# Kernel optimization log

Measured on AMD Instinct MI355X. Metric: run time of the kernel, lower is better.

## Reference

```python
import jax, jax.numpy as jnp
import numpy as np

D_MODEL = 1024
H = 16
D_K = D_MODEL // H
MAX_SEQ_LEN = 2048
B = 2
S = 2048


def setup_inputs() -> dict:
    key = jax.random.key(0)
    ks = jax.random.split(key, 8)
    scale = 1.0 / np.sqrt(D_MODEL)
    return {
        "q": jax.random.normal(ks[0], (B, S, D_MODEL), jnp.float32),
        "k": jax.random.normal(ks[1], (B, S, D_MODEL), jnp.float32),
        "v": jax.random.normal(ks[2], (B, S, D_MODEL), jnp.float32),
        "mask": jnp.ones((B, 1, S, S), dtype=bool),
        "w_q": jax.random.normal(ks[3], (D_MODEL, D_MODEL), jnp.float32) * scale,
        "w_k": jax.random.normal(ks[4], (D_MODEL, D_MODEL), jnp.float32) * scale,
        "w_v": jax.random.normal(ks[5], (D_MODEL, D_MODEL), jnp.float32) * scale,
        "w_o": jax.random.normal(ks[6], (D_MODEL, D_MODEL), jnp.float32) * scale,
        "rel_emb": jax.random.normal(ks[7], (2 * MAX_SEQ_LEN - 1, H), jnp.float32) * 0.02,
    }


def reference(q, k, v, mask, w_q, w_k, w_v, w_o, rel_emb):
    batch, seq_len, _ = q.shape
    # projections (nn.Linear without bias: x @ W.T)
    query = (q @ w_q.T).reshape(batch, seq_len, H, D_K).transpose(0, 2, 1, 3)
    key_ = (k @ w_k.T).reshape(batch, seq_len, H, D_K).transpose(0, 2, 1, 3)
    value = (v @ w_v.T).reshape(batch, seq_len, H, D_K).transpose(0, 2, 1, 3)
    # scores: [B, H, S, S]
    scores = jnp.einsum("bhqd,bhkd->bhqk", query, key_) / jnp.sqrt(jnp.float32(D_K))
    # relative position bias
    rng = jnp.arange(seq_len)
    rel_pos = rng[:, None] - rng[None, :] + (MAX_SEQ_LEN - 1)  # [S, S]
    rel_bias = rel_emb[rel_pos]                                # [S, S, H]
    scores = scores + rel_bias.transpose(2, 0, 1)[None]        # [1, H, S, S]
    scores = jnp.where(mask, scores, -1e9)
    attn = jax.nn.softmax(scores, axis=-1)  # dropout p=0 -> identity
    x = jnp.einsum("bhqk,bhkd->bhqd", attn, value)
    x = x.transpose(0, 2, 1, 3).reshape(batch, seq_len, H * D_K)
    return x @ w_o.T
```

## Files before the change

kernel.cpp:

```cpp
#include <hip/hip_runtime.h>
#include <hip/hip_bf16.h>
#include <stdint.h>

typedef __bf16 bf16_t;
typedef __bf16 bf16x8 __attribute__((ext_vector_type(8)));
typedef __bf16 bf16x4 __attribute__((ext_vector_type(4)));
typedef short  s16x4  __attribute__((ext_vector_type(4)));
typedef float  f32x4  __attribute__((ext_vector_type(4)));

#define D_MODEL 1024
#define NH 16
#define DK 64
#define SEQ 2048
#define BATCH 2
#define NKT (SEQ / 64)
#define LOG2E 1.44269504f

typedef const __attribute__((address_space(1))) void gas_void;
typedef __attribute__((address_space(3))) void las_void;
__device__ __forceinline__ void async16(const void* g, void* l) {
  __builtin_amdgcn_global_load_lds((gas_void*)g, (las_void*)l, 16, 0, 0);
}

__device__ __forceinline__ bf16x8 load8(const float* p) {
  float4 a = *(const float4*)p;
  float4 b = *(const float4*)(p + 4);
  bf16x8 r;
  r[0] = (bf16_t)a.x; r[1] = (bf16_t)a.y; r[2] = (bf16_t)a.z; r[3] = (bf16_t)a.w;
  r[4] = (bf16_t)b.x; r[5] = (bf16_t)b.y; r[6] = (bf16_t)b.z; r[7] = (bf16_t)b.w;
  return r;
}
__device__ __forceinline__ bf16x8 load8(const bf16_t* p) {
  return *(const bf16x8*)p;
}

__device__ __forceinline__ f32x4 mfma16x16x16_bf16(bf16x4 a, bf16x4 b, f32x4 c) {
#if __has_builtin(__builtin_amdgcn_mfma_f32_16x16x16_bf16)
  return __builtin_amdgcn_mfma_f32_16x16x16_bf16(a, b, c, 0, 0, 0);
#else
  union { bf16x4 h; s16x4 s; } ua, ub;
  ua.h = a; ub.h = b;
  return __builtin_amdgcn_mfma_f32_16x16x16bf16_1k(ua.s, ub.s, c, 0, 0, 0);
#endif
}

__global__ __launch_bounds__(256) void wcvt_kernel(
    const float* __restrict__ w0, const float* __restrict__ w1,
    const float* __restrict__ w2, const float* __restrict__ w3,
    bf16_t* __restrict__ o0, bf16_t* __restrict__ o1,
    bf16_t* __restrict__ o2, bf16_t* __restrict__ o3)
{
  const float* s; bf16_t* d;
  switch (blockIdx.y) {
    case 0:  s = w0; d = o0; break;
    case 1:  s = w1; d = o1; break;
    case 2:  s = w2; d = o2; break;
    default: s = w3; d = o3; break;
  }
  size_t i = (size_t)(blockIdx.x * 256 + threadIdx.x) * 8;
  *(bf16x8*)(d + i) = load8(s + i);
}

__global__ __launch_bounds__(256) void copy_kernel(
    const bf16_t* __restrict__ s, bf16_t* __restrict__ d)
{
  size_t i = (size_t)(blockIdx.x * 256 + threadIdx.x) * 8;
  *(bf16x8*)(d + i) = *(const bf16x8*)(s + i);
}

template <typename TA, typename TW>
__device__ __forceinline__ void gemm_mainloop_sync(const TA* __restrict__ A,
                                                   const TW* __restrict__ W,
                                                   int n0, int j0,
                                                   bf16_t* As, bf16_t* Ws,
                                                   f32x4 acc[4][4])
{
  const int tid  = threadIdx.x;
  const int wave = tid >> 6, lane = tid & 63;
  const int g = lane >> 4, rl = lane & 15;
  const int wm = (wave & 1) * 64, wn = (wave >> 1) * 64;

  for (int kt = 0; kt < D_MODEL / 64; ++kt) {
    __syncthreads();
#pragma unroll
    for (int i = 0; i < 4; ++i) {
      int c = tid + i * 256;
      int row = c >> 3, t = c & 7;
      *(bf16x8*)(As + row * 72 + t * 8) =
          load8(A + (size_t)(n0 + row) * D_MODEL + kt * 64 + t * 8);
      *(bf16x8*)(Ws + row * 72 + t * 8) =
          load8(W + (size_t)(j0 + row) * D_MODEL + kt * 64 + t * 8);
    }
    __syncthreads();
#pragma unroll
    for (int kc = 0; kc < 2; ++kc) {
      bf16x8 af[4], bfr[4];
#pragma unroll
      for (int mi = 0; mi < 4; ++mi)
        af[mi] = *(const bf16x8*)(As + (wm + mi * 16 + rl) * 72 + kc * 32 + g * 8);
#pragma unroll
      for (int ni = 0; ni < 4; ++ni)
        bfr[ni] = *(const bf16x8*)(Ws + (wn + ni * 16 + rl) * 72 + kc * 32 + g * 8);
#pragma unroll
      for (int mi = 0; mi < 4; ++mi)
#pragma unroll
        for (int ni = 0; ni < 4; ++ni)
          acc[mi][ni] = __builtin_amdgcn_mfma_f32_16x16x32_bf16(
              af[mi], bfr[ni], acc[mi][ni], 0, 0, 0);
    }
  }
}

__device__ __forceinline__ void qkv_epilogue(int which, int n0, int j0,
                                             f32x4 acc[4][4],
                                             bf16_t* qh, bf16_t* kh, bf16_t* vt)
{
  const int tid  = threadIdx.x;
  const int wave = tid >> 6, lane = tid & 63;
  const int g = lane >> 4, rl = lane & 15;
  const int wm = (wave & 1) * 64, wn = (wave >> 1) * 64;

  if (which == 2) {
    const int b = n0 >> 11;
#pragma unroll
    for (int mi = 0; mi < 4; ++mi)
#pragma unroll
      for (int ni = 0; ni < 4; ++ni) {
        bf16x4 pk;
#pragma unroll
        for (int r = 0; r < 4; ++r) pk[r] = (bf16_t)acc[mi][ni][r];
        int s = (n0 & (SEQ - 1)) + wm + mi * 16 + g * 4;
        int j = j0 + wn + ni * 16 + rl;
        int h = j >> 6, d = j & (DK - 1);
        int kl = s & 63;
        int n = ((kl >> 2) & 3) * 16 + ((kl >> 4) << 2);
        *(bf16x4*)(vt + ((((size_t)(b * NH + h) * NKT + (s >> 6)) * DK + d) << 6)
                   + n) = pk;
      }
  } else {
    bf16_t* O = (which == 0) ? qh : kh;
#pragma unroll
    for (int mi = 0; mi < 4; ++mi)
#pragma unroll
      for (int ni = 0; ni < 4; ++ni)
#pragma unroll
        for (int r = 0; r < 4; ++r) {
          int n = n0 + wm + mi * 16 + g * 4 + r;
          int j = j0 + wn + ni * 16 + rl;
          int b = n >> 11, s = n & (SEQ - 1);
          int h = j >> 6,  d = j & (DK - 1);
          O[((size_t)(b * NH + h) * SEQ + s) * DK + d] = (bf16_t)acc[mi][ni][r];
        }
  }
}

__global__ __launch_bounds__(256) void qkv_gemm_db2(
    const float* __restrict__ q, const float* __restrict__ k,
    const float* __restrict__ v,
    const bf16_t* __restrict__ wq, const bf16_t* __restrict__ wk,
    const bf16_t* __restrict__ wv,
    bf16_t* __restrict__ qh, bf16_t* __restrict__ kh, bf16_t* __restrict__ vt)
{
  __shared__ __align__(16) bf16_t smem[32768];

  const int bid   = blockIdx.x;
  const int lane8 = bid / 96;
  const int grp   = bid % 96;
  const int which = grp >> 5;
  const int nt    = grp & 31;
  const int j0 = lane8 * 128, n0 = nt * 128;

  const float*  A = (which == 0) ? q : (which == 1) ? k : v;
  const bf16_t* W = (which == 0) ? wq : (which == 1) ? wk : wv;

  const int tid  = threadIdx.x;
  const int wave = tid >> 6, lane = tid & 63;
  const int g = lane >> 4, rl = lane & 15;
  const int wm = (wave & 1) * 64, wn = (wave >> 1) * 64;
  const int row_ = tid >> 3, t_ = tid & 7;
  const int src_ = (t_ ^ (row_ & 7)) << 3;

  f32x4 pa[4], pb[4];
  f32x4 acc[4][4] = {};

  auto LOADA = [&](int kt) {
#pragma unroll
    for (int i = 0; i < 4; ++i) {
      const float* p = A + (size_t)(n0 + row_ + 32 * i) * D_MODEL + kt * 64 + t_ * 8;
      pa[i] = *(const f32x4*)p;
      pb[i] = *(const f32x4*)(p + 4);
    }
  };
  auto DMAW = [&](int kt, bf16_t* Wsb) {
#pragma unroll
    for (int i = 0; i < 4; ++i) {
      async16(W + (size_t)(j0 + row_ + 32 * i) * D_MODEL + kt * 64 + src_,
              Wsb + (tid + i * 256) * 8);
    }
  };
  auto WRITEA = [&](bf16_t* Asb) {
#pragma unroll
    for (int i = 0; i < 4; ++i) {
      bf16x8 h8;
#pragma unroll
      for (int r = 0; r < 4; ++r) {
        h8[r]     = (bf16_t)pa[i][r];
        h8[4 + r] = (bf16_t)pb[i][r];
      }
      *(bf16x8*)(Asb + (row_ + 32 * i) * 64 + src_) = h8;
    }
  };

  LOADA(0);
  DMAW(0, smem + 16384);
  WRITEA(smem);

  for (int kt = 0; kt < D_MODEL / 64; ++kt) {
    const int cur = kt & 1;
    if (kt + 1 < D_MODEL / 64) {
      LOADA(kt + 1);
      DMAW(kt + 1, smem + 16384 + (cur ^ 1) * 8192);
      asm volatile("s_waitcnt vmcnt(12) lgkmcnt(0)" ::: "memory");
    } else {
      asm volatile("s_waitcnt vmcnt(0) lgkmcnt(0)" ::: "memory");
    }
    __builtin_amdgcn_s_barrier();
    asm volatile("" ::: "memory");

    const bf16_t* Ab = smem + cur * 8192;
    const bf16_t* Wb = smem + 16384 + cur * 8192;
#pragma unroll
    for (int kc = 0; kc < 2; ++kc) {
      bf16x8 af[4], bfr[4];
      const int j8 = ((kc * 4 + g) ^ (rl & 7)) << 3;
#pragma unroll
      for (int mi = 0; mi < 4; ++mi)
        af[mi] = *(const bf16x8*)(Ab + (wm + mi * 16 + rl) * 64 + j8);
#pragma unroll
      for (int ni = 0; ni < 4; ++ni)
        bfr[ni] = *(const bf16x8*)(Wb + (wn + ni * 16 + rl) * 64 + j8);
      __builtin_amdgcn_s_setprio(1);
#pragma unroll
      for (int mi = 0; mi < 4; ++mi)
#pragma unroll
        for (int ni = 0; ni < 4; ++ni)
          acc[mi][ni] = __builtin_amdgcn_mfma_f32_16x16x32_bf16(
              af[mi], bfr[ni], acc[mi][ni], 0, 0, 0);
      __builtin_amdgcn_s_setprio(0);
    }

    if (kt + 1 < D_MODEL / 64) WRITEA(smem + (cur ^ 1) * 8192);
    asm volatile("s_waitcnt lgkmcnt(0)" ::: "memory");
    __builtin_amdgcn_s_barrier();
    asm volatile("" ::: "memory");
  }

  if (which == 2) {
    qkv_epilogue(2, n0, j0, acc, qh, kh, vt);
  } else {
    const int b = n0 >> 11, s0 = n0 & (SEQ - 1);
    bf16_t* O = (which == 0) ? qh : kh;
    __syncthreads();
    bf16_t* T = smem;
#pragma unroll
    for (int mi = 0; mi < 4; ++mi)
#pragma unroll
      for (int ni = 0; ni < 4; ++ni)
#pragma unroll
        for (int r = 0; r < 4; ++r)
          T[(wm + mi * 16 + g * 4 + r) * 136 + wn + ni * 16 + rl] =
              (bf16_t)acc[mi][ni][r];
    __syncthreads();
#pragma unroll
    for (int i = 0; i < 8; ++i) {
      int cc = tid + i * 256;
      int row = cc >> 4, t = cc & 15;
      int j = j0 + t * 8;
      int h = j >> 6, d = j & (DK - 1);
      *(bf16x8*)(O + ((size_t)(b * NH + h) * SEQ + s0 + row) * DK + d) =
          *(const bf16x8*)(T + row * 136 + t * 8);
    }
  }
}

__global__ __launch_bounds__(256) void qkv_gemm_sync(
    const float* __restrict__ q, const float* __restrict__ k,
    const float* __restrict__ v,
    const float* __restrict__ wq, const float* __restrict__ wk,
    const float* __restrict__ wv,
    bf16_t* __restrict__ qh, bf16_t* __restrict__ kh, bf16_t* __restrict__ vt)
{
  __shared__ __align__(16) bf16_t As[128 * 72];
  __shared__ __align__(16) bf16_t Ws[128 * 72];
  const int jt = blockIdx.x, nt = blockIdx.y;
  const int which = jt >> 3;
  const int j0 = (jt & 7) * 128, n0 = nt * 128;
  const float* A = (which == 0) ? q : (which == 1) ? k : v;
  const float* W = (which == 0) ? wq : (which == 1) ? wk : wv;
  f32x4 acc[4][4] = {};
  gemm_mainloop_sync(A, W, n0, j0, As, Ws, acc);
  qkv_epilogue(which, n0, j0, acc, qh, kh, vt);
}

__global__ __launch_bounds__(256) void attn_kernel(
    const bf16_t* __restrict__ qh, const bf16_t* __restrict__ kh,
    const bf16_t* __restrict__ vt, const float* __restrict__ rel,
    bf16_t* __restrict__ xa)
{
  __shared__ __align__(16) bf16_t Ks[2][4096];
  __shared__ __align__(16) bf16_t Vs[2][4096];
  __shared__ float relw[2176];

  const int bx = blockIdx.x;
  const int hb = bx & 31;
  const int qt = bx >> 5;
  const int h  = hb & (NH - 1);
  const int b  = hb >> 4;
  const int q0 = qt * 128;

  const size_t headoff = (size_t)(b * NH + h) * SEQ * DK;
  const bf16_t* Q  = qh + headoff;
  const bf16_t* K  = kh + headoff;
  const bf16_t* Vg = vt + headoff;

  const int tid  = threadIdx.x;
  const int wave = tid >> 6, lane = tid & 63;
  const int g = lane >> 4, rl = lane & 15;

  for (int t = tid; t < 2175; t += 256)
    relw[t] = rel[(size_t)(q0 + t) * NH + h] * LOG2E;

  bf16x8 aq[2][2];
#pragma unroll
  for (int mb = 0; mb < 2; ++mb) {
    const int qrow = q0 + wave * 32 + mb * 16 + rl;
    aq[mb][0] = *(const bf16x8*)(Q + (size_t)qrow * DK + g * 8);
    aq[mb][1] = *(const bf16x8*)(Q + (size_t)qrow * DK + 32 + g * 8);
  }

  bf16x4 ones4;
#pragma unroll
  for (int r = 0; r < 4; ++r) ones4[r] = (bf16_t)1.0f;

  f32x4 ls[2];
  ls[0] = (f32x4){0.f, 0.f, 0.f, 0.f};
  ls[1] = (f32x4){0.f, 0.f, 0.f, 0.f};
  f32x4 o[2][4];
#pragma unroll
  for (int mb = 0; mb < 2; ++mb)
#pragma unroll
    for (int nb = 0; nb < 4; ++nb) o[mb][nb] = (f32x4){0.f, 0.f, 0.f, 0.f};

  auto STAGE = [&](const bf16_t* Kt, const bf16_t* Vt, bf16_t* Kd, bf16_t* Vd) {
#pragma unroll
    for (int i = 0; i < 2; ++i) {
      int c = tid + i * 256;
      int pr  = c >> 7;
      int ph  = (c >> 6) & 1;
      int pg  = (c >> 4) & 3;
      int prl = c & 15;
      async16(Kt + (pr * 16 + prl) * 64 + ph * 32 + pg * 8, Kd + c * 8);
      async16(Vt + (pr * 16 + prl) * 64 + pg * 16 + ph * 8, Vd + c * 8);
    }
  };

  __syncthreads();

  STAGE(K, Vg, &Ks[0][0], &Vs[0][0]);

  for (int kt = 0; kt < NKT; ++kt) {
    const int cur = kt & 1;
    if (kt + 1 < NKT) {
      STAGE(K + (size_t)(kt + 1) * 4096, Vg + (size_t)(kt + 1) * 4096,
            &Ks[cur ^ 1][0], &Vs[cur ^ 1][0]);
      asm volatile("s_waitcnt vmcnt(4)" ::: "memory");
    } else {
      asm volatile("s_waitcnt vmcnt(0)" ::: "memory");
    }
    __builtin_amdgcn_s_barrier();
    asm volatile("" ::: "memory");

    const bf16_t* Kb = &Ks[cur][0];
    const bf16_t* Vb = &Vs[cur][0];

    bf16x8 kb0[4], kb1[4];
#pragma unroll
    for (int cb = 0; cb < 4; ++cb) {
      kb0[cb] = *(const bf16x8*)(Kb + (cb * 2 + 0) * 512 + lane * 8);
      kb1[cb] = *(const bf16x8*)(Kb + (cb * 2 + 1) * 512 + lane * 8);
    }
    bf16x8 vvf[4][2];
#pragma unroll
    for (int nb = 0; nb < 4; ++nb)
#pragma unroll
      for (int hf = 0; hf < 2; ++hf)
        vvf[nb][hf] = *(const bf16x8*)(Vb + (nb * 2 + hf) * 512 + lane * 8);

    const int base0 = wave * 32 + rl - g * 4 - kt * 64 + 2047;
    float rvw[5][4];
#pragma unroll
    for (int t5 = 0; t5 < 5; ++t5)
#pragma unroll
      for (int r = 0; r < 4; ++r)
        rvw[t5][r] = relw[base0 + (t5 - 3) * 16 - r];

    bf16x4 pf[2][4];
#pragma unroll
    for (int mb = 0; mb < 2; ++mb)
#pragma unroll
      for (int cb = 0; cb < 4; ++cb) {
        f32x4 a = (f32x4){0.f, 0.f, 0.f, 0.f};
        a = __builtin_amdgcn_mfma_f32_16x16x32_bf16(kb0[cb], aq[mb][0], a, 0, 0, 0);
        a = __builtin_amdgcn_mfma_f32_16x16x32_bf16(kb1[cb], aq[mb][1], a, 0, 0, 0);
        bf16x4 pk;
#pragma unroll
        for (int r = 0; r < 4; ++r)
          pk[r] = (bf16_t)__builtin_amdgcn_exp2f(
              fmaf(a[r], 0.125f * LOG2E, rvw[mb - cb + 3][r]));
        pf[mb][cb] = pk;
        ls[mb] = mfma16x16x16_bf16(pk, ones4, ls[mb]);
      }

    __builtin_amdgcn_s_setprio(1);
#pragma unroll
    for (int mb = 0; mb < 2; ++mb)
#pragma unroll
      for (int nb = 0; nb < 4; ++nb)
#pragma unroll
        for (int cb = 0; cb < 4; ++cb) {
          bf16x8 vv = vvf[nb][cb >> 1];
          bf16x4 v4;
#pragma unroll
          for (int r = 0; r < 4; ++r) v4[r] = vv[(cb & 1) * 4 + r];
          o[mb][nb] = mfma16x16x16_bf16(pf[mb][cb], v4, o[mb][nb]);
        }
    __builtin_amdgcn_s_setprio(0);

    __builtin_amdgcn_s_barrier();
  }

  float w2[2][4];
#pragma unroll
  for (int mb = 0; mb < 2; ++mb)
#pragma unroll
    for (int r = 0; r < 4; ++r) w2[mb][r] = 1.f / ls[mb][r];

#pragma unroll
  for (int mb = 0; mb < 2; ++mb)
#pragma unroll
    for (int nb = 0; nb < 4; ++nb)
#pragma unroll
      for (int r = 0; r < 4; ++r) {
        const int srow = q0 + wave * 32 + mb * 16 + g * 4 + r;
        const int d = nb * 16 + rl;
        xa[(size_t)(b * SEQ + srow) * D_MODEL + h * DK + d] =
            (bf16_t)(o[mb][nb][r] * w2[mb][r]);
      }
}

__device__ __forceinline__ void stage_out(
    const bf16_t* __restrict__ xa, const bf16_t* __restrict__ wo,
    int n0, int j0, int kt, bf16_t* Asb, bf16_t* Wsb, int tid)
{
#pragma unroll
  for (int i = 0; i < 2; ++i) {
    int c = tid + i * 256;
    int row = c >> 3, t = c & 7;
    int src = (t ^ (row & 7)) << 3;
    async16(xa + (size_t)(n0 + row) * D_MODEL + kt * 64 + src, Asb + c * 8);
  }
#pragma unroll
  for (int i = 0; i < 4; ++i) {
    int c = tid + i * 256;
    int row = c >> 3, t = c & 7;
    int src = (t ^ (row & 7)) << 3;
    async16(wo + (size_t)(j0 + row) * D_MODEL + kt * 64 + src, Wsb + c * 8);
  }
}

__global__ __launch_bounds__(256) void out_gemm_db(
    const bf16_t* __restrict__ xa, const bf16_t* __restrict__ wo,
    float* __restrict__ out)
{
  __shared__ __align__(16) bf16_t smem[24576];
  bf16_t* As = smem;
  bf16_t* Ws = smem + 8192;
  const int j0 = blockIdx.x * 128, n0 = blockIdx.y * 64;

  const int tid  = threadIdx.x;
  const int wave = tid >> 6, lane = tid & 63;
  const int g = lane >> 4, rl = lane & 15;
  const int wm = (wave & 1) * 32, wn = (wave >> 1) * 64;

  f32x4 acc[2][4] = {};
  stage_out(xa, wo, n0, j0, 0, As, Ws, tid);

  for (int kt = 0; kt < D_MODEL / 64; ++kt) {
    const int cur = kt & 1;
    if (kt + 1 < D_MODEL / 64) {
      stage_out(xa, wo, n0, j0, kt + 1, As + (cur ^ 1) * 4096,
                Ws + (cur ^ 1) * 8192, tid);
      asm volatile("s_waitcnt vmcnt(6)" ::: "memory");
    } else {
      asm volatile("s_waitcnt vmcnt(0)" ::: "memory");
    }
    __builtin_amdgcn_s_barrier();
    asm volatile("" ::: "memory");

    const bf16_t* Ab = As + cur * 4096;
    const bf16_t* Wb = Ws + cur * 8192;
#pragma unroll
    for (int kc = 0; kc < 2; ++kc) {
      bf16x8 af[2], bfr[4];
      const int j8 = ((kc * 4 + g) ^ (rl & 7)) << 3;
#pragma unroll
      for (int mi = 0; mi < 2; ++mi)
        af[mi] = *(const bf16x8*)(Ab + (wm + mi * 16 + rl) * 64 + j8);
#pragma unroll
      for (int ni = 0; ni < 4; ++ni)
        bfr[ni] = *(const bf16x8*)(Wb + (wn + ni * 16 + rl) * 64 + j8);
      __builtin_amdgcn_s_setprio(1);
#pragma unroll
      for (int mi = 0; mi < 2; ++mi)
#pragma unroll
        for (int ni = 0; ni < 4; ++ni)
          acc[mi][ni] = __builtin_amdgcn_mfma_f32_16x16x32_bf16(
              af[mi], bfr[ni], acc[mi][ni], 0, 0, 0);
      __builtin_amdgcn_s_setprio(0);
    }
    __builtin_amdgcn_s_barrier();
  }

#pragma unroll
  for (int mi = 0; mi < 2; ++mi)
#pragma unroll
    for (int ni = 0; ni < 4; ++ni)
#pragma unroll
      for (int r = 0; r < 4; ++r) {
        int n = n0 + wm + mi * 16 + g * 4 + r;
        int j = j0 + wn + ni * 16 + rl;
        out[(size_t)n * D_MODEL + j] = acc[mi][ni][r];
      }
}

__global__ __launch_bounds__(256) void out_gemm_sync(
    const bf16_t* __restrict__ xa, const float* __restrict__ wo,
    float* __restrict__ out)
{
  __shared__ __align__(16) bf16_t As[128 * 72];
  __shared__ __align__(16) bf16_t Ws[128 * 72];
  const int j0 = blockIdx.x * 128, n0 = blockIdx.y * 128;
  f32x4 acc[4][4] = {};
  gemm_mainloop_sync(xa, wo, n0, j0, As, Ws, acc);

  const int tid  = threadIdx.x;
  const int wave = tid >> 6, lane = tid & 63;
  const int g = lane >> 4, rl = lane & 15;
  const int wm = (wave & 1) * 64, wn = (wave >> 1) * 64;
#pragma unroll
  for (int mi = 0; mi < 4; ++mi)
#pragma unroll
    for (int ni = 0; ni < 4; ++ni)
#pragma unroll
      for (int r = 0; r < 4; ++r) {
        int n = n0 + wm + mi * 16 + g * 4 + r;
        int j = j0 + wn + ni * 16 + rl;
        out[(size_t)n * D_MODEL + j] = acc[mi][ni][r];
      }
}

extern "C" void kernel_launch(void* const* d_in, const int* in_sizes, int n_in,
                              void* d_out, int out_size, void* d_ws, size_t ws_size,
                              hipStream_t stream)
{
  const float* q   = (const float*)d_in[0];
  const float* k   = (const float*)d_in[1];
  const float* v   = (const float*)d_in[2];
  const float* wq  = (const float*)d_in[4];
  const float* wk  = (const float*)d_in[5];
  const float* wv  = (const float*)d_in[6];
  const float* wo  = (const float*)d_in[7];
  const float* rel = (const float*)d_in[8];
  float* out = (float*)d_out;

  char* ws = (char*)d_ws;
  const size_t seg  = (size_t)BATCH * SEQ * D_MODEL * sizeof(bf16_t);
  const size_t wseg = (size_t)D_MODEL * D_MODEL * sizeof(bf16_t);
  const size_t need = 4 * seg;

  if (ws_size >= need) {
    bf16_t* qh  = (bf16_t*)(ws);
    bf16_t* kh  = (bf16_t*)(ws + seg);
    bf16_t* vt  = (bf16_t*)(ws + 2 * seg);
    bf16_t* xa  = (bf16_t*)(ws + 3 * seg);
    bf16_t* wqb = (bf16_t*)d_out;
    bf16_t* wkb = (bf16_t*)((char*)d_out + wseg);
    bf16_t* wvb = (bf16_t*)((char*)d_out + 2 * wseg);
    bf16_t* wob = (bf16_t*)((char*)d_out + 3 * wseg);
    bf16_t* wos = qh;

    wcvt_kernel<<<dim3(512, 4), 256, 0, stream>>>(wq, wk, wv, wo,
                                                  wqb, wkb, wvb, wob);
    qkv_gemm_db2<<<dim3(768), 256, 0, stream>>>(q, k, v, wqb, wkb, wvb,
                                                qh, kh, vt);
    attn_kernel<<<dim3(512), 256, 0, stream>>>(qh, kh, vt, rel, xa);
    copy_kernel<<<dim3(512), 256, 0, stream>>>(wob, wos);
    out_gemm_db<<<dim3(8, 64), 256, 0, stream>>>(xa, wos, out);
  } else {
    bf16_t* qh = (bf16_t*)(ws);
    bf16_t* kh = (bf16_t*)(ws + seg);
    bf16_t* vt = (bf16_t*)(ws + 2 * seg);
    bf16_t* xa = (bf16_t*)(ws + 3 * seg);
    qkv_gemm_sync<<<dim3(24, 32), 256, 0, stream>>>(q, k, v, wq, wk, wv,
                                                    qh, kh, vt);
    attn_kernel<<<dim3(512), 256, 0, stream>>>(qh, kh, vt, rel, xa);
    out_gemm_sync<<<dim3(8, 32), 256, 0, stream>>>(xa, wo, out);
  }
}
```

Before: 247.6 us.

## Split attention key tiles across two waves per query group with LDS reduction

The attention kernel now runs 512 threads per block: each pair of waves shares a 32-row query group, and each wave in the pair handles half of every 64-key tile (intra-tile split-K). The partial output accumulators and row sums from the second wave go through shared memory (aliased onto the K/V buffers) and are added by the first wave before normalisation and store. This doubles the waves available for latency hiding and halves per-wave register use and MFMA work per tile. In exchange it adds two block-wide syncs and an LDS reduction at the end, and only half of the waves write output.

```diff
diff --git a/kernel.cpp b/kernel.cpp
--- a/kernel.cpp
+++ b/kernel.cpp
@@ -302,14 +302,16 @@
   qkv_epilogue(which, n0, j0, acc, qh, kh, vt);
 }
 
-__global__ __launch_bounds__(256) void attn_kernel(
+__global__ __launch_bounds__(512, 4) void attn_kernel(
     const bf16_t* __restrict__ qh, const bf16_t* __restrict__ kh,
     const bf16_t* __restrict__ vt, const float* __restrict__ rel,
     bf16_t* __restrict__ xa)
 {
-  __shared__ __align__(16) bf16_t Ks[2][4096];
-  __shared__ __align__(16) bf16_t Vs[2][4096];
-  __shared__ float relw[2176];
+  __shared__ __align__(16) char smem[41472];
+  bf16_t* Ks   = (bf16_t*)smem;
+  bf16_t* Vs   = (bf16_t*)(smem + 16384);
+  float*  relw = (float*)(smem + 32768);
+  float*  comb = (float*)smem;
 
   const int bx = blockIdx.x;
   const int hb = bx & 31;
@@ -324,16 +326,17 @@
   const bf16_t* Vg = vt + headoff;
 
   const int tid  = threadIdx.x;
-  const int wave = tid >> 6, lane = tid & 63;
+  const int w    = tid >> 6, lane = tid & 63;
+  const int qw   = w >> 1, kw = w & 1;
   const int g = lane >> 4, rl = lane & 15;
 
-  for (int t = tid; t < 2175; t += 256)
+  for (int t = tid; t < 2175; t += 512)
     relw[t] = rel[(size_t)(q0 + t) * NH + h] * LOG2E;
 
   bf16x8 aq[2][2];
 #pragma unroll
   for (int mb = 0; mb < 2; ++mb) {
-    const int qrow = q0 + wave * 32 + mb * 16 + rl;
+    const int qrow = q0 + qw * 32 + mb * 16 + rl;
     aq[mb][0] = *(const bf16x8*)(Q + (size_t)qrow * DK + g * 8);
     aq[mb][1] = *(const bf16x8*)(Q + (size_t)qrow * DK + 32 + g * 8);
   }
@@ -352,72 +355,68 @@
     for (int nb = 0; nb < 4; ++nb) o[mb][nb] = (f32x4){0.f, 0.f, 0.f, 0.f};
 
   auto STAGE = [&](const bf16_t* Kt, const bf16_t* Vt, bf16_t* Kd, bf16_t* Vd) {
-#pragma unroll
-    for (int i = 0; i < 2; ++i) {
-      int c = tid + i * 256;
-      int pr  = c >> 7;
-      int ph  = (c >> 6) & 1;
-      int pg  = (c >> 4) & 3;
-      int prl = c & 15;
-      async16(Kt + (pr * 16 + prl) * 64 + ph * 32 + pg * 8, Kd + c * 8);
-      async16(Vt + (pr * 16 + prl) * 64 + pg * 16 + ph * 8, Vd + c * 8);
-    }
+    int c = tid;
+    int pr  = c >> 7;
+    int ph  = (c >> 6) & 1;
+    int pg  = (c >> 4) & 3;
+    int prl = c & 15;
+    async16(Kt + (pr * 16 + prl) * 64 + ph * 32 + pg * 8, Kd + c * 8);
+    async16(Vt + (pr * 16 + prl) * 64 + pg * 16 + ph * 8, Vd + c * 8);
   };
 
   __syncthreads();
 
-  STAGE(K, Vg, &Ks[0][0], &Vs[0][0]);
+  STAGE(K, Vg, Ks, Vs);
 
   for (int kt = 0; kt < NKT; ++kt) {
     const int cur = kt & 1;
     if (kt + 1 < NKT) {
       STAGE(K + (size_t)(kt + 1) * 4096, Vg + (size_t)(kt + 1) * 4096,
-            &Ks[cur ^ 1][0], &Vs[cur ^ 1][0]);
-      asm volatile("s_waitcnt vmcnt(4)" ::: "memory");
+            Ks + (cur ^ 1) * 4096, Vs + (cur ^ 1) * 4096);
+      asm volatile("s_waitcnt vmcnt(2)" ::: "memory");
     } else {
       asm volatile("s_waitcnt vmcnt(0)" ::: "memory");
     }
     __builtin_amdgcn_s_barrier();
     asm volatile("" ::: "memory");
 
-    const bf16_t* Kb = &Ks[cur][0];
-    const bf16_t* Vb = &Vs[cur][0];
-
-    bf16x8 kb0[4], kb1[4];
-#pragma unroll
-    for (int cb = 0; cb < 4; ++cb) {
-      kb0[cb] = *(const bf16x8*)(Kb + (cb * 2 + 0) * 512 + lane * 8);
-      kb1[cb] = *(const bf16x8*)(Kb + (cb * 2 + 1) * 512 + lane * 8);
-    }
-    bf16x8 vvf[4][2];
+    const bf16_t* Kb = Ks + cur * 4096;
+    const bf16_t* Vb = Vs + cur * 4096;
+
+    bf16x8 kb0[2], kb1[2];
+#pragma unroll
+    for (int cb2 = 0; cb2 < 2; ++cb2) {
+      const int cb = kw * 2 + cb2;
+      kb0[cb2] = *(const bf16x8*)(Kb + (cb * 2 + 0) * 512 + lane * 8);
+      kb1[cb2] = *(const bf16x8*)(Kb + (cb * 2 + 1) * 512 + lane * 8);
+    }
+    bf16x8 vvf[4];
 #pragma unroll
     for (int nb = 0; nb < 4; ++nb)
-#pragma unroll
-      for (int hf = 0; hf < 2; ++hf)
-        vvf[nb][hf] = *(const bf16x8*)(Vb + (nb * 2 + hf) * 512 + lane * 8);
-
-    const int base0 = wave * 32 + rl - g * 4 - kt * 64 + 2047;
-    float rvw[5][4];
-#pragma unroll
-    for (int t5 = 0; t5 < 5; ++t5)
+      vvf[nb] = *(const bf16x8*)(Vb + (nb * 2 + kw) * 512 + lane * 8);
+
+    const int base0 = qw * 32 + rl - kt * 64 - kw * 32 - g * 4 + 2047;
+    float rvw[3][4];
+#pragma unroll
+    for (int t3 = 0; t3 < 3; ++t3)
 #pragma unroll
       for (int r = 0; r < 4; ++r)
-        rvw[t5][r] = relw[base0 + (t5 - 3) * 16 - r];
-
-    bf16x4 pf[2][4];
+        rvw[t3][r] = relw[base0 + (t3 - 1) * 16 - r];
+
+    bf16x4 pf[2][2];
 #pragma unroll
     for (int mb = 0; mb < 2; ++mb)
 #pragma unroll
-      for (int cb = 0; cb < 4; ++cb) {
+      for (int cb2 = 0; cb2 < 2; ++cb2) {
         f32x4 a = (f32x4){0.f, 0.f, 0.f, 0.f};
-        a = __builtin_amdgcn_mfma_f32_16x16x32_bf16(kb0[cb], aq[mb][0], a, 0, 0, 0);
-        a = __builtin_amdgcn_mfma_f32_16x16x32_bf16(kb1[cb], aq[mb][1], a, 0, 0, 0);
+        a = __builtin_amdgcn_mfma_f32_16x16x32_bf16(kb0[cb2], aq[mb][0], a, 0, 0, 0);
+        a = __builtin_amdgcn_mfma_f32_16x16x32_bf16(kb1[cb2], aq[mb][1], a, 0, 0, 0);
         bf16x4 pk;
 #pragma unroll
         for (int r = 0; r < 4; ++r)
           pk[r] = (bf16_t)__builtin_amdgcn_exp2f(
-              fmaf(a[r], 0.125f * LOG2E, rvw[mb - cb + 3][r]));
-        pf[mb][cb] = pk;
+              fmaf(a[r], 0.125f * LOG2E, rvw[mb - cb2 + 1][r]));
+        pf[mb][cb2] = pk;
         ls[mb] = mfma16x16x16_bf16(pk, ones4, ls[mb]);
       }
 
@@ -427,35 +426,62 @@
 #pragma unroll
       for (int nb = 0; nb < 4; ++nb)
 #pragma unroll
-        for (int cb = 0; cb < 4; ++cb) {
-          bf16x8 vv = vvf[nb][cb >> 1];
+        for (int cb2 = 0; cb2 < 2; ++cb2) {
           bf16x4 v4;
 #pragma unroll
-          for (int r = 0; r < 4; ++r) v4[r] = vv[(cb & 1) * 4 + r];
-          o[mb][nb] = mfma16x16x16_bf16(pf[mb][cb], v4, o[mb][nb]);
+          for (int r = 0; r < 4; ++r) v4[r] = vvf[nb][cb2 * 4 + r];
+          o[mb][nb] = mfma16x16x16_bf16(pf[mb][cb2], v4, o[mb][nb]);
         }
     __builtin_amdgcn_s_setprio(0);
 
     __builtin_amdgcn_s_barrier();
   }
 
-  float w2[2][4];
-#pragma unroll
-  for (int mb = 0; mb < 2; ++mb)
-#pragma unroll
-    for (int r = 0; r < 4; ++r) w2[mb][r] = 1.f / ls[mb][r];
-
-#pragma unroll
-  for (int mb = 0; mb < 2; ++mb)
-#pragma unroll
-    for (int nb = 0; nb < 4; ++nb)
-#pragma unroll
-      for (int r = 0; r < 4; ++r) {
-        const int srow = q0 + wave * 32 + mb * 16 + g * 4 + r;
-        const int d = nb * 16 + rl;
-        xa[(size_t)(b * SEQ + srow) * D_MODEL + h * DK + d] =
-            (bf16_t)(o[mb][nb][r] * w2[mb][r]);
+  __syncthreads();
+  if (kw == 1) {
+    float* dst = comb + ((size_t)qw * 64 + lane) * 40;
+#pragma unroll
+    for (int mb = 0; mb < 2; ++mb)
+#pragma unroll
+      for (int nb = 0; nb < 4; ++nb)
+        *(f32x4*)(dst + (mb * 4 + nb) * 4) = o[mb][nb];
+    *(f32x4*)(dst + 32) = ls[0];
+    *(f32x4*)(dst + 36) = ls[1];
+  }
+  __syncthreads();
+  if (kw == 0) {
+    const float* src = comb + ((size_t)qw * 64 + lane) * 40;
+#pragma unroll
+    for (int mb = 0; mb < 2; ++mb)
+#pragma unroll
+      for (int nb = 0; nb < 4; ++nb) {
+        f32x4 p = *(const f32x4*)(src + (mb * 4 + nb) * 4);
+#pragma unroll
+        for (int r = 0; r < 4; ++r) o[mb][nb][r] += p[r];
       }
+    f32x4 l0 = *(const f32x4*)(src + 32);
+    f32x4 l1 = *(const f32x4*)(src + 36);
+#pragma unroll
+    for (int r = 0; r < 4; ++r) { ls[0][r] += l0[r]; ls[1][r] += l1[r]; }
+
+    float w2[2][4];
+#pragma unroll
+    for (int mb = 0; mb < 2; ++mb)
+#pragma unroll
+      for (int r = 0; r < 4; ++r) w2[mb][r] = 1.f / ls[mb][r];
+
+#pragma unroll
+    for (int mb = 0; mb < 2; ++mb)
+#pragma unroll
+      for (int nb = 0; nb < 4; ++nb)
+#pragma unroll
+        for (int r = 0; r < 4; ++r) {
+          const int srow = q0 + qw * 32 + mb * 16 + g * 4 + r;
+          const int d = nb * 16 + rl;
+          xa[(size_t)(b * SEQ + srow) * D_MODEL + h * DK + d] =
+              (bf16_t)(o[mb][nb][r] * w2[mb][r]);
+        }
+  }
 }
 
 __device__ __forceinline__ void stage_out(
@@ -603,7 +629,7 @@
                                                   wqb, wkb, wvb, wob);
     qkv_gemm_db2<<<dim3(768), 256, 0, stream>>>(q, k, v, wqb, wkb, wvb,
                                                 qh, kh, vt);
-    attn_kernel<<<dim3(512), 256, 0, stream>>>(qh, kh, vt, rel, xa);
+    attn_kernel<<<dim3(512), 512, 0, stream>>>(qh, kh, vt, rel, xa);
     copy_kernel<<<dim3(512), 256, 0, stream>>>(wob, wos);
     out_gemm_db<<<dim3(8, 64), 256, 0, stream>>>(xa, wos, out);
   } else {
@@ -613,7 +639,7 @@
     bf16_t* xa = (bf16_t*)(ws + 3 * seg);
     qkv_gemm_sync<<<dim3(24, 32), 256, 0, stream>>>(q, k, v, wq, wk, wv,
                                                     qh, kh, vt);
-    attn_kernel<<<dim3(512), 256, 0, stream>>>(qh, kh, vt, rel, xa);
+    attn_kernel<<<dim3(512), 512, 0, stream>>>(qh, kh, vt, rel, xa);
     out_gemm_sync<<<dim3(8, 32), 256, 0, stream>>>(xa, wo, out);
   }
 }
```

After: 241.9 us. -2.3%, faster.
